# Optimization experiments

Measured on AMD Instinct MI355X. Metric: run time of the kernel, lower is better.

## Reference

```python
import jax, jax.numpy as jnp
import numpy as np
import math

EPS_NORM = 1e-6
EPS_COS = 1e-6


def _rms_norm(x, scale, eps):
    ms = jnp.mean(jnp.square(x), axis=-1, keepdims=True)
    return x * (scale * jax.lax.rsqrt(ms + eps))


def _apply_rope(x, theta):
    # x: [n, nh, s, e], theta: [n, nh, s, d] with 2*d <= e
    d = theta.shape[-1]
    x1, x2, rest = x[..., :d], x[..., d:2 * d], x[..., 2 * d:]
    cos, sin = jnp.cos(theta), jnp.sin(theta)
    y1 = x1 * cos - x2 * sin
    y2 = x2 * cos + x1 * sin
    return jnp.concatenate([y1, y2, rest], axis=-1)


def _make_freqs(d_head, n_heads):
    dim = d_head // 2
    log_min, log_max = math.log(math.pi), math.log(10.0 * math.pi)
    f = np.exp(np.linspace(log_min, log_max, n_heads * dim // 4 + 1, dtype=np.float64)[:-1])
    return jnp.asarray(f.reshape(dim // 4, n_heads).T, dtype=jnp.float32)  # [n_heads, dim//4]


def setup_inputs() -> dict:
    key = jax.random.key(0)
    ks = jax.random.split(key, 8)
    n, H, W, d_model = 4, 32, 32, 1024
    d_head, n_heads, cond_f = 64, 16, 1024
    x = jax.random.normal(ks[0], (n, H, W, d_model), dtype=jnp.float32)
    pos = jax.random.uniform(ks[1], (n, H, W, 2), dtype=jnp.float32) * 2.0 - 1.0
    cond = jax.random.normal(ks[2], (n, cond_f), dtype=jnp.float32)
    norm_scale = jnp.ones((d_model,), dtype=jnp.float32)
    ada_w = jax.random.normal(ks[3], (3 * d_model, cond_f), dtype=jnp.float32) * 0.02
    ada_b = jnp.zeros((3 * d_model,), dtype=jnp.float32)
    qkv_w = jax.random.normal(ks[4], (3 * d_model, d_model), dtype=jnp.float32) * 0.02
    attn_scale = jnp.full((n_heads,), 10.0, dtype=jnp.float32)
    out_w = jax.random.normal(ks[5], (d_model, d_model), dtype=jnp.float32) * 0.02
    freqs = _make_freqs(d_head, n_heads)
    return {"x": x, "pos": pos, "cond": cond, "norm_scale": norm_scale,
            "ada_w": ada_w, "ada_b": ada_b, "qkv_w": qkv_w,
            "attn_scale": attn_scale, "out_w": out_w, "freqs": freqs}


def reference(x, pos, cond, norm_scale, ada_w, ada_b, qkv_w, attn_scale, out_w, freqs):
    n, H, W, d_model = x.shape
    n_heads, nf = freqs.shape          # nf = d_head//4... actually (d_head//2)//4
    d_head = d_model // n_heads
    s = H * W
    skip = x
    # adaLN modulation
    mod = jax.nn.silu(cond) @ ada_w.T + ada_b              # [n, 3*d_model]
    shift, scale, gate = jnp.split(mod, 3, axis=-1)        # each [n, d_model]
    xn = _rms_norm(x, norm_scale, EPS_NORM)
    xm = xn * (1.0 + scale[:, None, None, :]) + shift[:, None, None, :]
    # qkv projection: layout (t nh e) on last dim
    qkv = (xm @ qkv_w.T).reshape(n, s, 3, n_heads, d_head)
    q, k, v = qkv[:, :, 0], qkv[:, :, 1], qkv[:, :, 2]     # [n, s, nh, e]
    q = jnp.transpose(q, (0, 2, 1, 3))                     # [n, nh, s, e]
    k = jnp.transpose(k, (0, 2, 1, 3))
    v = jnp.transpose(v, (0, 2, 1, 3))
    # cosine-sim scaling per head
    sqrt_scale = jnp.sqrt(attn_scale)[None, :, None, None]
    q = q * (sqrt_scale * jax.lax.rsqrt(jnp.sum(jnp.square(q), axis=-1, keepdims=True) + EPS_COS))
    k = k * (sqrt_scale * jax.lax.rsqrt(jnp.sum(jnp.square(k), axis=-1, keepdims=True) + EPS_COS))
    # axial RoPE angles
    posf = pos.reshape(n, s, 2)
    theta_h = posf[:, :, None, 0:1] * freqs                # [n, s, nh, nf]
    theta_w = posf[:, :, None, 1:2] * freqs
    theta = jnp.concatenate([theta_h, theta_w], axis=-1)   # [n, s, nh, 2*nf]
    theta = jnp.transpose(theta, (0, 2, 1, 3))             # [n, nh, s, 2*nf]
    q = _apply_rope(q, theta)
    k = _apply_rope(k, theta)
    # attention with softmax scale 1.0 (cosine-sim already scaled)
    scores = jnp.einsum('bnse,bnte->bnst', q, k)
    attn = jax.nn.softmax(scores, axis=-1)
    o = jnp.einsum('bnst,bnte->bnse', attn, v)             # [n, nh, s, e]
    o = jnp.transpose(o, (0, 2, 1, 3)).reshape(n, H, W, d_model)
    o = o @ out_w.T
    return skip + gate[:, None, None, :] * o
```

## Files before the change

### kernel.cpp

```cpp
#include <hip/hip_runtime.h>
#include <stdint.h>

typedef __bf16 bf16x8 __attribute__((ext_vector_type(8)));
typedef uint16_t u16x8 __attribute__((ext_vector_type(8)));
typedef float f32x4 __attribute__((ext_vector_type(4)));

#define DEV static __device__ __forceinline__

DEV uint16_t f2bf(float f) {
  union { float f; uint32_t u; } v; v.f = f;
  return (uint16_t)((v.u + 0x8000u) >> 16);
}
DEV float bf2f(uint16_t h) {
  union { uint32_t u; float f; } v; v.u = ((uint32_t)h) << 16;
  return v.f;
}

#define GLOAD_LDS16(g, l)                                                     \
  __builtin_amdgcn_global_load_lds(                                           \
      (__attribute__((address_space(1))) void*)(g),                           \
      (__attribute__((address_space(3))) void*)(l), 16, 0, 0)

__global__ void k_conv(const float* __restrict__ src, uint16_t* __restrict__ dst, int n) {
  int i = blockIdx.x * blockDim.x + threadIdx.x;
  int stride = gridDim.x * blockDim.x;
  for (; i < n; i += stride) dst[i] = f2bf(src[i]);
}

__global__ void k_mod(const float* __restrict__ cond, const float* __restrict__ ada_w,
                      const float* __restrict__ ada_b, float* __restrict__ mod) {
  int w = threadIdx.x >> 6, lane = threadIdx.x & 63;
  int gid = blockIdx.x * 4 + w;
  int b = gid / 3072, j = gid - b * 3072;
  const float* cw = cond + b * 1024;
  const float* aw = ada_w + (size_t)j * 1024;
  float sum = 0.f;
  for (int i = 0; i < 16; ++i) {
    int f = lane + (i << 6);
    float c = cw[f];
    float sc = c / (1.f + __expf(-c));
    sum += sc * aw[f];
  }
  for (int m = 32; m; m >>= 1) sum += __shfl_xor(sum, m, 64);
  if (lane == 0) mod[b * 3072 + j] = sum + ada_b[j];
}

__global__ void k_norm_mod(const float* __restrict__ x, const float* __restrict__ norm_scale,
                           const float* __restrict__ mod, uint16_t* __restrict__ xm) {
  int row = blockIdx.x;
  int b = row >> 10;
  const float* xr = x + (size_t)row * 1024;
  const float* shiftp = mod + b * 3072;
  const float* scalep = shiftp + 1024;
  int t = threadIdx.x;
  float v[4];
  float s = 0.f;
  for (int i = 0; i < 4; ++i) { v[i] = xr[t + (i << 8)]; s += v[i] * v[i]; }
  for (int m = 32; m; m >>= 1) s += __shfl_xor(s, m, 64);
  __shared__ float red[4];
  if ((t & 63) == 0) red[t >> 6] = s;
  __syncthreads();
  s = red[0] + red[1] + red[2] + red[3];
  float inv = rsqrtf(s * (1.f / 1024.f) + 1e-6f);
  uint16_t* xo = xm + (size_t)row * 1024;
  for (int i = 0; i < 4; ++i) {
    int c = t + (i << 8);
    float val = v[i] * inv * norm_scale[c];
    val = val * (1.f + scalep[c]) + shiftp[c];
    xo[c] = f2bf(val);
  }
}

template <int N, int EPI>
__global__ __launch_bounds__(256) void k_gemm(const uint16_t* __restrict__ A,
                                              const uint16_t* __restrict__ B,
                                              uint16_t* __restrict__ Cbf,
                                              const float* __restrict__ skip,
                                              const float* __restrict__ modp,
                                              float* __restrict__ Cout) {
  constexpr int K = 1024;
  __shared__ uint16_t As[128 * 32];
  __shared__ uint16_t Bs[128 * 32];
  int t = threadIdx.x;
  int lane = t & 63;
  int w = t >> 6, wr = w >> 1, wc = w & 1;
  int bm = blockIdx.y, bn = blockIdx.x;
  f32x4 acc[4][4] = {};
  const size_t a_base = (size_t)(bm * 128) * K;
  const size_t b_base = (size_t)(bn * 128) * K;
  int r = t >> 2, c8 = (t & 3) << 3;
  for (int kt = 0; kt < K / 32; ++kt) {
    __syncthreads();
    for (int i = 0; i < 2; ++i) {
      int rr = r + (i << 6);
      GLOAD_LDS16(A + a_base + (size_t)rr * K + kt * 32 + c8, As + rr * 32 + c8);
      GLOAD_LDS16(B + b_base + (size_t)rr * K + kt * 32 + c8, Bs + rr * 32 + c8);
    }
    __syncthreads();
    bf16x8 af[4], bfr[4];
    int klo = (lane >> 4) << 3;
    for (int m = 0; m < 4; ++m)
      af[m] = *reinterpret_cast<const bf16x8*>(&As[(wr * 64 + m * 16 + (lane & 15)) * 32 + klo]);
    for (int n = 0; n < 4; ++n)
      bfr[n] = *reinterpret_cast<const bf16x8*>(&Bs[(wc * 64 + n * 16 + (lane & 15)) * 32 + klo]);
    for (int m = 0; m < 4; ++m)
      for (int n = 0; n < 4; ++n)
        acc[m][n] = __builtin_amdgcn_mfma_f32_16x16x32_bf16(af[m], bfr[n], acc[m][n], 0, 0, 0);
  }
  int row0 = bm * 128 + wr * 64;
  int col0 = bn * 128 + wc * 64;
  for (int m = 0; m < 4; ++m)
    for (int n = 0; n < 4; ++n)
      for (int rr = 0; rr < 4; ++rr) {
        int R = row0 + m * 16 + ((lane >> 4) << 2) + rr;
        int C = col0 + n * 16 + (lane & 15);
        float v = acc[m][n][rr];
        if (EPI == 0) {
          Cbf[(size_t)R * N + C] = f2bf(v);
        } else {
          float g = modp[(R >> 10) * 3072 + 2048 + C];
          Cout[(size_t)R * N + C] = skip[(size_t)R * N + C] + g * v;
        }
      }
}

__global__ __launch_bounds__(256) void k_qkvpost(
    const uint16_t* __restrict__ qkv, const float* __restrict__ pos,
    const float* __restrict__ freqs, const float* __restrict__ attn_scale,
    uint16_t* __restrict__ Qb, uint16_t* __restrict__ Kb, uint16_t* __restrict__ Vt) {
  __shared__ uint16_t vtile[64 * 66];
  int t = threadIdx.x;
  int st = blockIdx.x, bh = blockIdx.y;
  int b = bh >> 4, h = bh & 15;
  int r = t >> 2;
  int s = t & 3;
  int sp = st * 64 + r;
  size_t m = (size_t)b * 1024 + sp;
  const uint16_t* basep = qkv + m * 3072 + h * 64 + s * 16;
  bf16x8 q0 = *reinterpret_cast<const bf16x8*>(basep);
  bf16x8 q1 = *reinterpret_cast<const bf16x8*>(basep + 8);
  bf16x8 k0 = *reinterpret_cast<const bf16x8*>(basep + 1024);
  bf16x8 k1 = *reinterpret_cast<const bf16x8*>(basep + 1032);
  u16x8 v0 = *reinterpret_cast<const u16x8*>(basep + 2048);
  u16x8 v1 = *reinterpret_cast<const u16x8*>(basep + 2056);
  float qv[16], kv[16];
#pragma unroll
  for (int i = 0; i < 8; ++i) {
    qv[i] = (float)q0[i]; qv[8 + i] = (float)q1[i];
    kv[i] = (float)k0[i]; kv[8 + i] = (float)k1[i];
  }
  float sq = 0.f, sk = 0.f;
#pragma unroll
  for (int i = 0; i < 16; ++i) { sq += qv[i] * qv[i]; sk += kv[i] * kv[i]; }
  sq += __shfl_xor(sq, 1, 64); sq += __shfl_xor(sq, 2, 64);
  sk += __shfl_xor(sk, 1, 64); sk += __shfl_xor(sk, 2, 64);
  float ss = sqrtf(attn_scale[h]);
  float qs = ss * rsqrtf(sq + 1e-6f);
  float ks = ss * rsqrtf(sk + 1e-6f);
#pragma unroll
  for (int i = 0; i < 16; ++i) { qv[i] *= qs; kv[i] *= ks; }
  float p0 = pos[m * 2], p1 = pos[m * 2 + 1];
  float sgn = (s == 0) ? -1.f : 1.f;
#pragma unroll
  for (int i = 0; i < 16; ++i) {
    float pq = __shfl_xor(qv[i], 1, 64);
    float pk = __shfl_xor(kv[i], 1, 64);
    if (s < 2) {
      float th = ((i < 8) ? p0 : p1) * freqs[h * 8 + (i & 7)];
      float sn, cs;
      __sincosf(th, &sn, &cs);
      qv[i] = qv[i] * cs + sgn * pq * sn;
      kv[i] = kv[i] * cs + sgn * pk * sn;
    }
  }
  bf16x8 qo0, qo1, ko0, ko1;
#pragma unroll
  for (int i = 0; i < 8; ++i) {
    qo0[i] = (__bf16)qv[i]; qo1[i] = (__bf16)qv[8 + i];
    ko0[i] = (__bf16)kv[i]; ko1[i] = (__bf16)kv[8 + i];
  }
  size_t qkb = ((size_t)bh * 1024 + sp) * 64 + s * 16;
  *reinterpret_cast<bf16x8*>(Qb + qkb) = qo0;
  *reinterpret_cast<bf16x8*>(Qb + qkb + 8) = qo1;
  *reinterpret_cast<bf16x8*>(Kb + qkb) = ko0;
  *reinterpret_cast<bf16x8*>(Kb + qkb + 8) = ko1;
#pragma unroll
  for (int i = 0; i < 8; ++i) {
    vtile[(s * 16 + i) * 66 + r] = v0[i];
    vtile[(s * 16 + 8 + i) * 66 + r] = v1[i];
  }
  __syncthreads();
  int d = t >> 2, c = t & 3;
  u16x8 w0, w1;
#pragma unroll
  for (int i = 0; i < 8; ++i) {
    w0[i] = vtile[d * 66 + c * 16 + i];
    w1[i] = vtile[d * 66 + c * 16 + 8 + i];
  }
  size_t vb = ((size_t)bh * 64 + d) * 1024 + st * 64 + c * 16;
  *reinterpret_cast<u16x8*>(Vt + vb) = w0;
  *reinterpret_cast<u16x8*>(Vt + vb + 8) = w1;
}

__global__ __launch_bounds__(512) void k_attn(const uint16_t* __restrict__ Qb,
                                              const uint16_t* __restrict__ Kb,
                                              const uint16_t* __restrict__ Vt,
                                              uint16_t* __restrict__ obuf) {
  __shared__ uint16_t Ks[64 * 64];
  __shared__ uint16_t Vs[64 * 64];
  __shared__ uint16_t Ps[8][16 * 88];
  int t = threadIdx.x, lane = t & 63, w = t >> 6;
  int qt = blockIdx.y, bh = blockIdx.x;
  int b = bh >> 4, h = bh & 15;
  int qrow = qt * 128 + w * 16 + (lane & 15);
  int klo = (lane >> 4) << 3;
  const uint16_t* qptr = Qb + ((size_t)bh * 1024 + qrow) * 64 + klo;
  bf16x8 qf0 = *reinterpret_cast<const bf16x8*>(qptr);
  bf16x8 qf1 = *reinterpret_cast<const bf16x8*>(qptr + 32);
  f32x4 oacc[4] = {};
  float denom[4] = {0.f, 0.f, 0.f, 0.f};
  const size_t kbase = (size_t)bh * 1024 * 64;
  const size_t vbase = (size_t)bh * 64 * 1024;
  for (int kt = 0; kt < 16; ++kt) {
    __syncthreads();
    {
      int row = t >> 3;
      int ce = ((t & 7) ^ (row & 7)) << 3;
      GLOAD_LDS16(Kb + kbase + (size_t)(kt * 64 + row) * 64 + ce, Ks + t * 8);
      GLOAD_LDS16(Vt + vbase + (size_t)row * 1024 + kt * 64 + ce, Vs + t * 8);
    }
    __syncthreads();
    bf16x8 pa0, pa1;
    {
      f32x4 s[4];
      for (int n = 0; n < 4; ++n) {
        int row = n * 16 + (lane & 15);
        int sw = (row & 7) << 3;
        bf16x8 kf0 = *reinterpret_cast<const bf16x8*>(&Ks[row * 64 + (klo ^ sw)]);
        bf16x8 kf1 = *reinterpret_cast<const bf16x8*>(&Ks[row * 64 + ((32 + klo) ^ sw)]);
        f32x4 z = {};
        z = __builtin_amdgcn_mfma_f32_16x16x32_bf16(qf0, kf0, z, 0, 0, 0);
        z = __builtin_amdgcn_mfma_f32_16x16x32_bf16(qf1, kf1, z, 0, 0, 0);
        s[n] = z;
      }
      for (int n = 0; n < 4; ++n)
        for (int rr = 0; rr < 4; ++rr) {
          float p = __expf(s[n][rr]);
          denom[rr] += p;
          Ps[w][(((lane >> 4) << 2) + rr) * 88 + n * 16 + (lane & 15)] = f2bf(p);
        }
      pa0 = *reinterpret_cast<const bf16x8*>(&Ps[w][(lane & 15) * 88 + klo]);
      pa1 = *reinterpret_cast<const bf16x8*>(&Ps[w][(lane & 15) * 88 + 32 + klo]);
    }
    for (int dt = 0; dt < 4; ++dt) {
      int row = dt * 16 + (lane & 15);
      int sw = (row & 7) << 3;
      bf16x8 vf0 = *reinterpret_cast<const bf16x8*>(&Vs[row * 64 + (klo ^ sw)]);
      bf16x8 vf1 = *reinterpret_cast<const bf16x8*>(&Vs[row * 64 + ((32 + klo) ^ sw)]);
      oacc[dt] = __builtin_amdgcn_mfma_f32_16x16x32_bf16(pa0, vf0, oacc[dt], 0, 0, 0);
      oacc[dt] = __builtin_amdgcn_mfma_f32_16x16x32_bf16(pa1, vf1, oacc[dt], 0, 0, 0);
    }
  }
  for (int rr = 0; rr < 4; ++rr)
    for (int msk = 8; msk; msk >>= 1) denom[rr] += __shfl_xor(denom[rr], msk, 64);
  for (int rr = 0; rr < 4; ++rr) {
    float rinv = 1.f / denom[rr];
    int sp = qt * 128 + w * 16 + ((lane >> 4) << 2) + rr;
    size_t orow = ((size_t)b * 1024 + sp) * 1024 + h * 64;
    for (int dt = 0; dt < 4; ++dt)
      obuf[orow + dt * 16 + (lane & 15)] = f2bf(oacc[dt][rr] * rinv);
  }
}

extern "C" void kernel_launch(void* const* d_in, const int* in_sizes, int n_in,
                              void* d_out, int out_size, void* d_ws, size_t ws_size,
                              hipStream_t stream) {
  const float* x = (const float*)d_in[0];
  const float* pos = (const float*)d_in[1];
  const float* cond = (const float*)d_in[2];
  const float* norm_scale = (const float*)d_in[3];
  const float* ada_w = (const float*)d_in[4];
  const float* ada_b = (const float*)d_in[5];
  const float* qkv_w = (const float*)d_in[6];
  const float* attn_scale = (const float*)d_in[7];
  const float* out_w = (const float*)d_in[8];
  const float* freqs = (const float*)d_in[9];
  float* out = (float*)d_out;
  char* ws = (char*)d_ws;
  float* mod = (float*)(ws + 0);
  uint16_t* xm = (uint16_t*)(ws + 65536);
  uint16_t* qkvw_bf = (uint16_t*)(ws + 8454144);
  uint16_t* outw_bf = (uint16_t*)(ws + 14745600);
  uint16_t* qkv = (uint16_t*)(ws + 16842752);
  uint16_t* Qb = (uint16_t*)(ws + 42008576);
  uint16_t* Kb = (uint16_t*)(ws + 50397184);
  uint16_t* Vt = (uint16_t*)(ws + 58785792);
  uint16_t* obuf = (uint16_t*)(ws + 67174400);

  k_conv<<<dim3(1024), dim3(256), 0, stream>>>(qkv_w, qkvw_bf, 3 * 1024 * 1024);
  k_conv<<<dim3(512), dim3(256), 0, stream>>>(out_w, outw_bf, 1024 * 1024);
  k_mod<<<dim3(3072), dim3(256), 0, stream>>>(cond, ada_w, ada_b, mod);
  k_norm_mod<<<dim3(4096), dim3(256), 0, stream>>>(x, norm_scale, mod, xm);
  k_gemm<3072, 0><<<dim3(24, 32), dim3(256), 0, stream>>>(xm, qkvw_bf, qkv, nullptr, nullptr, nullptr);
  k_qkvpost<<<dim3(16, 64), dim3(256), 0, stream>>>(qkv, pos, freqs, attn_scale, Qb, Kb, Vt);
  k_attn<<<dim3(64, 8), dim3(512), 0, stream>>>(Qb, Kb, Vt, obuf);
  k_gemm<1024, 1><<<dim3(8, 32), dim3(256), 0, stream>>>(obuf, outw_bf, nullptr, x, mod, out);
}
```

Before: 125.8 us.

## Double-buffer GEMM LDS tiles with K=64 steps, XOR swizzle and block remap

Reworks the bf16 GEMM main loop so the global-to-LDS load of the next K tile overlaps the MFMA work on the current one, using two LDS buffers and a single barrier per iteration. The K step grows from 32 to 64, the LDS layout is XOR-swizzled to reduce bank conflicts on fragment reads, and workgroups are remapped in an 8-way swizzle to improve L2 reuse. LDS use grows to 64 KB per block, which may reduce occupancy.

```diff
diff --git a/kernel.cpp b/kernel.cpp
--- a/kernel.cpp
+++ b/kernel.cpp
@@ -79,38 +79,78 @@
                                               const float* __restrict__ modp,
                                               float* __restrict__ Cout) {
   constexpr int K = 1024;
-  __shared__ uint16_t As[128 * 32];
-  __shared__ uint16_t Bs[128 * 32];
+  constexpr int NKT = K / 64;
+  __shared__ uint16_t As[2][128 * 64];
+  __shared__ uint16_t Bs[2][128 * 64];
   int t = threadIdx.x;
   int lane = t & 63;
   int w = t >> 6, wr = w >> 1, wc = w & 1;
-  int bm = blockIdx.y, bn = blockIdx.x;
+  int gx = gridDim.x;
+  int nwg = gx * gridDim.y;
+  int flat = blockIdx.y * gx + blockIdx.x;
+  int swz = (flat & 7) * (nwg >> 3) + (flat >> 3);
+  int bm = swz / gx, bn = swz % gx;
   f32x4 acc[4][4] = {};
   const size_t a_base = (size_t)(bm * 128) * K;
   const size_t b_base = (size_t)(bn * 128) * K;
-  int r = t >> 2, c8 = (t & 3) << 3;
-  for (int kt = 0; kt < K / 32; ++kt) {
+
+  int sr = t >> 3, sc = t & 7;
+#define STAGE(pb, kt)                                                          \
+  _Pragma("unroll") for (int i = 0; i < 4; ++i) {                              \
+    int rr = (i << 5) + sr;                                                    \
+    int cc = (sc ^ (rr & 7)) << 3;                                             \
+    GLOAD_LDS16(A + a_base + (size_t)rr * K + (kt) * 64 + cc,                  \
+                &As[pb][(rr << 6) + (sc << 3)]);                               \
+    GLOAD_LDS16(B + b_base + (size_t)rr * K + (kt) * 64 + cc,                  \
+                &Bs[pb][(rr << 6) + (sc << 3)]);                               \
+  }
+
+  STAGE(0, 0);
+  __syncthreads();
+
+  int lq = lane >> 4;
+  for (int kt = 0; kt < NKT; ++kt) {
+    int cur = kt & 1;
+    if (kt < NKT - 1) STAGE(cur ^ 1, kt + 1);
+    bf16x8 af[4][2], bfr[4][2];
+#pragma unroll
+    for (int m = 0; m < 4; ++m) {
+      int R = wr * 64 + m * 16 + (lane & 15);
+      int base = (R << 6);
+      int s8 = R & 7;
+#pragma unroll
+      for (int kh = 0; kh < 2; ++kh)
+        af[m][kh] = *reinterpret_cast<const bf16x8*>(
+            &As[cur][base + ((((kh << 2) + lq) ^ s8) << 3)]);
+    }
+#pragma unroll
+    for (int n = 0; n < 4; ++n) {
+      int R = wc * 64 + n * 16 + (lane & 15);
+      int base = (R << 6);
+      int s8 = R & 7;
+#pragma unroll
+      for (int kh = 0; kh < 2; ++kh)
+        bfr[n][kh] = *reinterpret_cast<const bf16x8*>(
+            &Bs[cur][base + ((((kh << 2) + lq) ^ s8) << 3)]);
+    }
+#pragma unroll
+    for (int m = 0; m < 4; ++m)
+#pragma unroll
+      for (int n = 0; n < 4; ++n) {
+        acc[m][n] = __builtin_amdgcn_mfma_f32_16x16x32_bf16(af[m][0], bfr[n][0], acc[m][n], 0, 0, 0);
+        acc[m][n] = __builtin_amdgcn_mfma_f32_16x16x32_bf16(af[m][1], bfr[n][1], acc[m][n], 0, 0, 0);
+      }
     __syncthreads();
-    for (int i = 0; i < 2; ++i) {
-      int rr = r + (i << 6);
-      GLOAD_LDS16(A + a_base + (size_t)rr * K + kt * 32 + c8, As + rr * 32 + c8);
-      GLOAD_LDS16(B + b_base + (size_t)rr * K + kt * 32 + c8, Bs + rr * 32 + c8);
-    }
-    __syncthreads();
-    bf16x8 af[4], bfr[4];
-    int klo = (lane >> 4) << 3;
-    for (int m = 0; m < 4; ++m)
-      af[m] = *reinterpret_cast<const bf16x8*>(&As[(wr * 64 + m * 16 + (lane & 15)) * 32 + klo]);
-    for (int n = 0; n < 4; ++n)
-      bfr[n] = *reinterpret_cast<const bf16x8*>(&Bs[(wc * 64 + n * 16 + (lane & 15)) * 32 + klo]);
-    for (int m = 0; m < 4; ++m)
-      for (int n = 0; n < 4; ++n)
-        acc[m][n] = __builtin_amdgcn_mfma_f32_16x16x32_bf16(af[m], bfr[n], acc[m][n], 0, 0, 0);
-  }
+  }
+#undef STAGE
+
   int row0 = bm * 128 + wr * 64;
   int col0 = bn * 128 + wc * 64;
+#pragma unroll
   for (int m = 0; m < 4; ++m)
+#pragma unroll
     for (int n = 0; n < 4; ++n)
+#pragma unroll
       for (int rr = 0; rr < 4; ++rr) {
         int R = row0 + m * 16 + ((lane >> 4) << 2) + rr;
         int C = col0 + n * 16 + (lane & 15);
```

After: 134.9 us. 1.07x slower.
